# Performance work log

Measured on AMD Instinct MI355X. Metric: run time of the kernel, lower is better.

Reference implementation:

```python
import jax, jax.numpy as jnp
import numpy as np

ENCODED_DIM = 64
NUM_ENCODED = 512
BETA = 0.25


def setup_inputs() -> dict:
    key = jax.random.key(0)
    k1, k2 = jax.random.split(key)
    inputs = jax.random.normal(k1, (32, 64, 64, ENCODED_DIM), dtype=jnp.float32)
    # tf.random_uniform_initializer default: U[-0.05, 0.05]
    codebook = jax.random.uniform(k2, (ENCODED_DIM, NUM_ENCODED), dtype=jnp.float32,
                                  minval=-0.05, maxval=0.05)
    return {"inputs": inputs, "codebook": codebook}


def reference(inputs, codebook):
    original_shape = inputs.shape
    flat = inputs.reshape(-1, ENCODED_DIM)  # [N, D]
    # Squared Euclidean distances to each codebook column: [N, K]
    norms = (jnp.sum(flat ** 2, axis=1, keepdims=True)
             + jnp.sum(codebook ** 2, axis=0)
             - 2.0 * flat @ codebook)
    idx = jnp.argmin(norms, axis=1)  # [N]
    # one_hot @ codebook.T is exactly a row-gather of codebook.T
    quantized = jnp.take(codebook.T, idx, axis=0).reshape(original_shape)
    quantized_loss = jnp.mean((quantized - jax.lax.stop_gradient(inputs)) ** 2)
    commitment_loss = jnp.mean((jax.lax.stop_gradient(quantized) - inputs) ** 2)
    loss = BETA * commitment_loss + quantized_loss
    out = inputs + jax.lax.stop_gradient(quantized - inputs)
    return out, loss
```

## Files before the change

### kernel.cpp

```cpp
#include <hip/hip_runtime.h>
#include <math.h>

#define D 64
#define K 512
#define ROWS 131072
#define NELEM (ROWS * D)
#define TGAP 64.0f
#define FLAGBIT (1 << 30)

typedef _Float16 half8 __attribute__((ext_vector_type(8)));
typedef float floatx4 __attribute__((ext_vector_type(4)));


__global__ __launch_bounds__(512) void vq_setup(const float* __restrict__ cb,
                                                _Float16* __restrict__ gH,
                                                _Float16* __restrict__ gL,
                                                float* __restrict__ Bn) {
    int idx = blockIdx.x * 512 + threadIdx.x;
    int k = idx >> 9, n = idx & 511;
    float c = cb[idx];
    float t = c * 4096.0f;
    _Float16 ch = (_Float16)t;
    float r = t - (float)ch;
    _Float16 cl = (_Float16)(r * 4096.0f);
    int off = (((n >> 4) * 2 + (k >> 5)) * 64 + ((k >> 3) & 3) * 16 + (n & 15)) * 8 + (k & 7);
    gH[off] = ch;
    gL[off] = cl;
    if (blockIdx.x == 0) {
#pragma clang fp contract(off)
        int j = threadIdx.x;
        float b = 0.f;
        for (int kk = 0; kk < D; ++kk) { float cc = cb[kk * K + j]; b = b + cc * cc; }
        Bn[j] = b * 0x1p20f;
    }
}

__global__ __launch_bounds__(256, 2) void vq_main(const float* __restrict__ x,
                                                  const float* __restrict__ cb,
                                                  const _Float16* __restrict__ gH,
                                                  const _Float16* __restrict__ gL,
                                                  const float* __restrict__ Bn,
                                                  float* __restrict__ out,
                                                  double* __restrict__ loss_acc,
                                                  unsigned int* __restrict__ bitmap) {
    __shared__ float ldsB[K];
    __shared__ int rowinfo[4][64];
    __shared__ unsigned int flagbits[8];
    __shared__ float wavesum[4];

    const int tid = threadIdx.x;
    const int lane = tid & 63;
    const int w = tid >> 6;
    const int quad = lane >> 4;
    const int nn = lane & 15;

    ldsB[tid] = Bn[tid];
    ldsB[tid + 256] = Bn[tid + 256];
    if (tid < 8) flagbits[tid] = 0;

    const int rowBase = blockIdx.x * 256 + w * 64;

    half8 xh[4][2], xl[4][2];
    #pragma unroll
    for (int tt = 0; tt < 4; ++tt) {
        #pragma unroll
        for (int s = 0; s < 2; ++s) {
            const float* xp = x + (size_t)(rowBase + tt * 16 + nn) * D + s * 32 + quad * 8;
            float4 v0 = *(const float4*)xp;
            float4 v1 = *(const float4*)(xp + 4);
            float vv[8] = {v0.x, v0.y, v0.z, v0.w, v1.x, v1.y, v1.z, v1.w};
            #pragma unroll
            for (int j = 0; j < 8; ++j) {
                float t = vv[j] * 256.0f;
                _Float16 h = (_Float16)t;
                float r = t - (float)h;
                xh[tt][s][j] = h;
                xl[tt][s][j] = (_Float16)(r * 4096.0f);
            }
        }
    }
    __syncthreads();

    float m1[4][4], m2[4][4];
    int   i1[4][4];
    #pragma unroll
    for (int tt = 0; tt < 4; ++tt)
        #pragma unroll
        for (int r = 0; r < 4; ++r) { m1[tt][r] = INFINITY; m2[tt][r] = INFINITY; i1[tt][r] = 0; }

    const half8* bHp = (const half8*)gH;
    const half8* bLp = (const half8*)gL;

    #pragma unroll 2
    for (int t = 0; t < 32; ++t) {
        half8 bh0 = bHp[(t * 2 + 0) * 64 + lane];
        half8 bl0 = bLp[(t * 2 + 0) * 64 + lane];
        half8 bh1 = bHp[(t * 2 + 1) * 64 + lane];
        half8 bl1 = bLp[(t * 2 + 1) * 64 + lane];
        int col = t * 16 + nn;
        float Bj = ldsB[col];
        #pragma unroll
        for (int tt = 0; tt < 4; ++tt) {
            floatx4 a1 = {0.f, 0.f, 0.f, 0.f};
            floatx4 a2 = {0.f, 0.f, 0.f, 0.f};
            a2 = __builtin_amdgcn_mfma_f32_16x16x32_f16(xl[tt][0], bh0, a2, 0, 0, 0);
            a2 = __builtin_amdgcn_mfma_f32_16x16x32_f16(xh[tt][0], bl0, a2, 0, 0, 0);
            a1 = __builtin_amdgcn_mfma_f32_16x16x32_f16(xh[tt][0], bh0, a1, 0, 0, 0);
            a2 = __builtin_amdgcn_mfma_f32_16x16x32_f16(xl[tt][1], bh1, a2, 0, 0, 0);
            a2 = __builtin_amdgcn_mfma_f32_16x16x32_f16(xh[tt][1], bl1, a2, 0, 0, 0);
            a1 = __builtin_amdgcn_mfma_f32_16x16x32_f16(xh[tt][1], bh1, a1, 0, 0, 0);
            #pragma unroll
            for (int r = 0; r < 4; ++r) {
                float macc = fmaf(0x1p-12f, a2[r], a1[r]);
                float g = fmaf(-2.0f, macc, Bj);
                float old1 = m1[tt][r];
                bool c1 = g < old1;
                m2[tt][r] = fminf(fmaxf(g, old1), m2[tt][r]);
                m1[tt][r] = c1 ? g : old1;
                i1[tt][r] = c1 ? col : i1[tt][r];
            }
        }
    }

    #pragma unroll
    for (int dlt = 1; dlt < 16; dlt <<= 1) {
        #pragma unroll
        for (int tt = 0; tt < 4; ++tt)
            #pragma unroll
            for (int r = 0; r < 4; ++r) {
                float om1 = __shfl_xor(m1[tt][r], dlt);
                int   oi1 = __shfl_xor(i1[tt][r], dlt);
                float om2 = __shfl_xor(m2[tt][r], dlt);
                bool ofirst = (om1 < m1[tt][r]) || (om1 == m1[tt][r] && oi1 < i1[tt][r]);
                float l1   = ofirst ? m1[tt][r] : om1;
                float cand = ofirst ? om2 : m2[tt][r];
                m1[tt][r] = ofirst ? om1 : m1[tt][r];
                i1[tt][r] = ofirst ? oi1 : i1[tt][r];
                m2[tt][r] = fminf(cand, l1);
            }
    }

    if (nn == 0) {
        #pragma unroll
        for (int tt = 0; tt < 4; ++tt)
            #pragma unroll
            for (int r = 0; r < 4; ++r) {
                int rl = tt * 16 + quad * 4 + r;
                bool flg = (m2[tt][r] - m1[tt][r]) < TGAP;
                rowinfo[w][rl] = i1[tt][r] | (flg ? FLAGBIT : 0);
                if (flg) atomicOr(&flagbits[(w * 64 + rl) >> 5], 1u << ((w * 64 + rl) & 31));
            }
    }
    __syncthreads();
    if (tid < 8) bitmap[blockIdx.x * 8 + tid] = flagbits[tid];

    float lsum = 0.f;
    #pragma unroll
    for (int tt = 0; tt < 4; ++tt) {
        #pragma unroll
        for (int p = 0; p < 4; ++p) {
            int rl = tt * 16 + p * 4 + quad;
            int info = rowinfo[w][rl];
            if (!(info & FLAGBIT)) {
                int j = info & 511;
                int kb = nn * 4;
                float q0 = cb[(kb + 0) * K + j];
                float q1 = cb[(kb + 1) * K + j];
                float q2 = cb[(kb + 2) * K + j];
                float q3 = cb[(kb + 3) * K + j];
                size_t row = (size_t)rowBase + rl;
                float4 xv = *(const float4*)(x + row * D + kb);
                float e0 = q0 - xv.x, e1 = q1 - xv.y, e2 = q2 - xv.z, e3 = q3 - xv.w;
                lsum += e0 * e0 + e1 * e1 + e2 * e2 + e3 * e3;
                *(float4*)(out + row * D + kb) = make_float4(q0, q1, q2, q3);
            }
        }
    }
    #pragma unroll
    for (int off = 32; off > 0; off >>= 1) lsum += __shfl_down(lsum, off);
    if (lane == 0) wavesum[w] = lsum;
    __syncthreads();
    if (tid == 0) {
        double tot = (double)wavesum[0] + (double)wavesum[1]
                   + (double)wavesum[2] + (double)wavesum[3];
        atomicAdd(loss_acc, tot);
    }
}

__global__ __launch_bounds__(256) void vq_rescan(const float* __restrict__ x,
                                                 const float* __restrict__ cb,
                                                 float* __restrict__ out,
                                                 double* __restrict__ loss_acc,
                                                 const unsigned int* __restrict__ bitmap) {
#pragma clang fp contract(off)
    const int lane = threadIdx.x & 63;
    const int gwave = blockIdx.x * 4 + (threadIdx.x >> 6);

    unsigned int w0 = bitmap[gwave * 2 + 0];
    unsigned int w1 = bitmap[gwave * 2 + 1];
    unsigned long long mask = ((unsigned long long)w1 << 32) | w0;
    float wloss = 0.f;
    if (mask) {
        float bn[8];
        #pragma unroll
        for (int m = 0; m < 8; ++m) bn[m] = 0.f;
        for (int k = 0; k < D; ++k) {
            const float* crow = cb + k * K + lane;
            #pragma unroll
            for (int m = 0; m < 8; ++m) {
                float c = crow[m * 64];
                bn[m] = bn[m] + c * c;
            }
        }
        while (mask) {
            int b = __builtin_ctzll(mask);
            mask &= mask - 1;
            int row = gwave * 64 + b;
            const float* xr = x + (size_t)row * D;
            float A0;
            {
                float rr[8];
                #pragma unroll
                for (int l = 0; l < 8; ++l) rr[l] = xr[l] * xr[l];
                #pragma unroll
                for (int m = 1; m < 8; ++m)
                    #pragma unroll
                    for (int l = 0; l < 8; ++l) {
                        float q = xr[8 * m + l] * xr[8 * m + l];
                        rr[l] = rr[l] + q;
                    }
                A0 = ((rr[0] + rr[1]) + (rr[2] + rr[3])) + ((rr[4] + rr[5]) + (rr[6] + rr[7]));
            }
            float a[8];
            #pragma unroll
            for (int m = 0; m < 8; ++m) a[m] = 0.f;
            for (int k = 0; k < D; ++k) {
                float xk = xr[k];
                const float* crow = cb + k * K + lane;
                #pragma unroll
                for (int m = 0; m < 8; ++m)
                    a[m] = fmaf(xk, crow[m * 64], a[m]);
            }
            float db = INFINITY; int jb = 0x7fffffff;
            #pragma unroll
            for (int m = 0; m < 8; ++m) {
                float s = A0 + bn[m];
                float t2 = 2.0f * a[m];
                float d = s - t2;
                int j = lane + (m << 6);
                if (d < db) { db = d; jb = j; }
            }
            for (int s = 1; s < 64; s <<= 1) {
                float od = __shfl_xor(db, s);
                int oj = __shfl_xor(jb, s);
                if ((od < db) || (od == db && oj < jb)) { db = od; jb = oj; }
            }
            float q = cb[lane * K + jb];
            out[(size_t)row * D + lane] = q;
            float e = q - xr[lane];
            wloss += e * e;
        }
    }
    #pragma unroll
    for (int off = 32; off > 0; off >>= 1) wloss += __shfl_down(wloss, off);
    if (lane == 0 && wloss != 0.f) atomicAdd(loss_acc, (double)wloss);
}

__global__ void vq_finalize(const double* __restrict__ acc, float* __restrict__ out) {
    out[NELEM] = (float)(acc[0] * (1.25 / (double)NELEM));
}

extern "C" void kernel_launch(void* const* d_in, const int* in_sizes, int n_in,
                              void* d_out, int out_size, void* d_ws, size_t ws_size,
                              hipStream_t stream) {
    const float* x  = (const float*)d_in[0];
    const float* cb = (const float*)d_in[1];
    float* out = (float*)d_out;
    double* loss_acc = (double*)d_ws;
    float* Bn        = (float*)((char*)d_ws + 4096);
    _Float16* gH     = (_Float16*)((char*)d_ws + 8192);
    _Float16* gL     = (_Float16*)((char*)d_ws + 73728);
    unsigned int* bm = (unsigned int*)((char*)d_ws + 139264);

    hipMemsetAsync(d_ws, 0, 16, stream);
    vq_setup<<<64, 512, 0, stream>>>(cb, gH, gL, Bn);
    vq_main<<<ROWS / 256, 256, 0, stream>>>(x, cb, gH, gL, Bn, out, loss_acc, bm);
    vq_rescan<<<512, 256, 0, stream>>>(x, cb, out, loss_acc, bm);
    vq_finalize<<<1, 1, 0, stream>>>(loss_acc, out);
}
```

Baseline: 176.7 us.

## Fuse rescan and finalize into main VQ kernel with packed-index max argmin

Removes the separate rescan and finalize kernels and the memset. Each block now re-checks its own ambiguous rows in-block, and the last block to finish, tracked by an atomic counter, writes the loss. The argmin becomes a max over negated distances, with the bias preloaded into the MFMA accumulator and the column index packed into the low mantissa bits, which drops the separate index and compare registers. Blocks shrink to 128 rows with higher occupancy (launch bounds 4). In exchange, the rescan work is serialized on wave 0 of each block, and the packed index loses 9 mantissa bits of distance precision, which the widened gap threshold has to cover.

```diff
diff --git a/kernel.cpp b/kernel.cpp
--- a/kernel.cpp
+++ b/kernel.cpp
@@ -5,7 +5,8 @@
 #define K 512
 #define ROWS 131072
 #define NELEM (ROWS * D)
-#define TGAP 64.0f
+#define NBLOCKS 1024
+#define TGAP_ACC 640.0f
 #define FLAGBIT (1 << 30)
 
 typedef _Float16 half8 __attribute__((ext_vector_type(8)));
@@ -15,14 +16,16 @@
 __global__ __launch_bounds__(512) void vq_setup(const float* __restrict__ cb,
                                                 _Float16* __restrict__ gH,
                                                 _Float16* __restrict__ gL,
-                                                float* __restrict__ Bn) {
+                                                float* __restrict__ Bneg,
+                                                double* __restrict__ loss,
+                                                int* __restrict__ done) {
     int idx = blockIdx.x * 512 + threadIdx.x;
     int k = idx >> 9, n = idx & 511;
     float c = cb[idx];
     float t = c * 4096.0f;
     _Float16 ch = (_Float16)t;
     float r = t - (float)ch;
-    _Float16 cl = (_Float16)(r * 4096.0f);
+    _Float16 cl = (_Float16)r;
     int off = (((n >> 4) * 2 + (k >> 5)) * 64 + ((k >> 3) & 3) * 16 + (n & 15)) * 8 + (k & 7);
     gH[off] = ch;
     gL[off] = cl;
@@ -31,21 +34,72 @@
         int j = threadIdx.x;
         float b = 0.f;
         for (int kk = 0; kk < D; ++kk) { float cc = cb[kk * K + j]; b = b + cc * cc; }
-        Bn[j] = b * 0x1p20f;
-    }
-}
-
-__global__ __launch_bounds__(256, 2) void vq_main(const float* __restrict__ x,
+        Bneg[j] = b * -0x1p19f;
+        if (j == 0) { *loss = 0.0; *done = 0; }
+    }
+}
+
+__device__ __noinline__ void exact_row(int row, const float* __restrict__ x,
+                                       const float* __restrict__ cb,
+                                       const float* bn, int lane,
+                                       float* __restrict__ out, float& lsum) {
+#pragma clang fp contract(off)
+    const float* xr = x + (size_t)row * D;
+    float A0;
+    {
+        float rr[8];
+        #pragma unroll
+        for (int l = 0; l < 8; ++l) rr[l] = xr[l] * xr[l];
+        #pragma unroll
+        for (int m = 1; m < 8; ++m)
+            #pragma unroll
+            for (int l = 0; l < 8; ++l) {
+                float q = xr[8 * m + l] * xr[8 * m + l];
+                rr[l] = rr[l] + q;
+            }
+        A0 = ((rr[0] + rr[1]) + (rr[2] + rr[3])) + ((rr[4] + rr[5]) + (rr[6] + rr[7]));
+    }
+    float a[8];
+    #pragma unroll
+    for (int m = 0; m < 8; ++m) a[m] = 0.f;
+    for (int k = 0; k < D; ++k) {
+        float xk = xr[k];
+        const float* crow = cb + k * K + lane;
+        #pragma unroll
+        for (int m = 0; m < 8; ++m)
+            a[m] = fmaf(xk, crow[m * 64], a[m]);
+    }
+    float db = INFINITY; int jb = 0x7fffffff;
+    #pragma unroll
+    for (int m = 0; m < 8; ++m) {
+        float s = A0 + bn[m];
+        float t2 = 2.0f * a[m];
+        float d = s - t2;
+        int j = lane + (m << 6);
+        if (d < db) { db = d; jb = j; }
+    }
+    for (int s = 1; s < 64; s <<= 1) {
+        float od = __shfl_xor(db, s);
+        int oj = __shfl_xor(jb, s);
+        if ((od < db) || (od == db && oj < jb)) { db = od; jb = oj; }
+    }
+    float q = cb[lane * K + jb];
+    out[(size_t)row * D + lane] = q;
+    float e = q - xr[lane];
+    lsum += e * e;
+}
+
+__global__ __launch_bounds__(256, 4) void vq_main(const float* __restrict__ x,
                                                   const float* __restrict__ cb,
                                                   const _Float16* __restrict__ gH,
                                                   const _Float16* __restrict__ gL,
-                                                  const float* __restrict__ Bn,
+                                                  const float* __restrict__ BnegG,
                                                   float* __restrict__ out,
                                                   double* __restrict__ loss_acc,
-                                                  unsigned int* __restrict__ bitmap) {
+                                                  int* __restrict__ done) {
     __shared__ float ldsB[K];
-    __shared__ int rowinfo[4][64];
-    __shared__ unsigned int flagbits[8];
+    __shared__ int rowinfo[4][32];
+    __shared__ unsigned int flagbits[4];
     __shared__ float wavesum[4];
 
     const int tid = threadIdx.x;
@@ -54,15 +108,15 @@
     const int quad = lane >> 4;
     const int nn = lane & 15;
 
-    ldsB[tid] = Bn[tid];
-    ldsB[tid + 256] = Bn[tid + 256];
-    if (tid < 8) flagbits[tid] = 0;
-
-    const int rowBase = blockIdx.x * 256 + w * 64;
-
-    half8 xh[4][2], xl[4][2];
-    #pragma unroll
-    for (int tt = 0; tt < 4; ++tt) {
+    ldsB[tid] = BnegG[tid];
+    ldsB[tid + 256] = BnegG[tid + 256];
+    if (tid < 4) flagbits[tid] = 0;
+
+    const int rowBase = blockIdx.x * 128 + w * 32;
+
+    half8 xh[2][2], xl[2][2];
+    #pragma unroll
+    for (int tt = 0; tt < 2; ++tt) {
         #pragma unroll
         for (int s = 0; s < 2; ++s) {
             const float* xp = x + (size_t)(rowBase + tt * 16 + nn) * D + s * 32 + quad * 8;
@@ -75,18 +129,17 @@
                 _Float16 h = (_Float16)t;
                 float r = t - (float)h;
                 xh[tt][s][j] = h;
-                xl[tt][s][j] = (_Float16)(r * 4096.0f);
+                xl[tt][s][j] = (_Float16)r;
             }
         }
     }
     __syncthreads();
 
-    float m1[4][4], m2[4][4];
-    int   i1[4][4];
-    #pragma unroll
-    for (int tt = 0; tt < 4; ++tt)
-        #pragma unroll
-        for (int r = 0; r < 4; ++r) { m1[tt][r] = INFINITY; m2[tt][r] = INFINITY; i1[tt][r] = 0; }
+    float M1[2][4], M2[2][4];
+    #pragma unroll
+    for (int tt = 0; tt < 2; ++tt)
+        #pragma unroll
+        for (int r = 0; r < 4; ++r) { M1[tt][r] = -INFINITY; M2[tt][r] = -INFINITY; }
 
     const half8* bHp = (const half8*)gH;
     const half8* bLp = (const half8*)gL;
@@ -97,27 +150,23 @@
         half8 bl0 = bLp[(t * 2 + 0) * 64 + lane];
         half8 bh1 = bHp[(t * 2 + 1) * 64 + lane];
         half8 bl1 = bLp[(t * 2 + 1) * 64 + lane];
-        int col = t * 16 + nn;
-        float Bj = ldsB[col];
-        #pragma unroll
-        for (int tt = 0; tt < 4; ++tt) {
-            floatx4 a1 = {0.f, 0.f, 0.f, 0.f};
-            floatx4 a2 = {0.f, 0.f, 0.f, 0.f};
-            a2 = __builtin_amdgcn_mfma_f32_16x16x32_f16(xl[tt][0], bh0, a2, 0, 0, 0);
-            a2 = __builtin_amdgcn_mfma_f32_16x16x32_f16(xh[tt][0], bl0, a2, 0, 0, 0);
-            a1 = __builtin_amdgcn_mfma_f32_16x16x32_f16(xh[tt][0], bh0, a1, 0, 0, 0);
-            a2 = __builtin_amdgcn_mfma_f32_16x16x32_f16(xl[tt][1], bh1, a2, 0, 0, 0);
-            a2 = __builtin_amdgcn_mfma_f32_16x16x32_f16(xh[tt][1], bl1, a2, 0, 0, 0);
-            a1 = __builtin_amdgcn_mfma_f32_16x16x32_f16(xh[tt][1], bh1, a1, 0, 0, 0);
+        float bneg = ldsB[t * 16 + nn];
+        unsigned int colbits = (unsigned)(t * 16 + nn);
+        #pragma unroll
+        for (int tt = 0; tt < 2; ++tt) {
+            floatx4 acc = {bneg, bneg, bneg, bneg};
+            acc = __builtin_amdgcn_mfma_f32_16x16x32_f16(xh[tt][0], bh0, acc, 0, 0, 0);
+            acc = __builtin_amdgcn_mfma_f32_16x16x32_f16(xl[tt][0], bh0, acc, 0, 0, 0);
+            acc = __builtin_amdgcn_mfma_f32_16x16x32_f16(xh[tt][0], bl0, acc, 0, 0, 0);
+            acc = __builtin_amdgcn_mfma_f32_16x16x32_f16(xh[tt][1], bh1, acc, 0, 0, 0);
+            acc = __builtin_amdgcn_mfma_f32_16x16x32_f16(xl[tt][1], bh1, acc, 0, 0, 0);
+            acc = __builtin_amdgcn_mfma_f32_16x16x32_f16(xh[tt][1], bl1, acc, 0, 0, 0);
             #pragma unroll
             for (int r = 0; r < 4; ++r) {
-                float macc = fmaf(0x1p-12f, a2[r], a1[r]);
-                float g = fmaf(-2.0f, macc, Bj);
-                float old1 = m1[tt][r];
-                bool c1 = g < old1;
-                m2[tt][r] = fminf(fmaxf(g, old1), m2[tt][r]);
-                m1[tt][r] = c1 ? g : old1;
-                i1[tt][r] = c1 ? col : i1[tt][r];
+                float gq = __uint_as_float((__float_as_uint(acc[r]) & ~511u) | colbits);
+                float lo = fminf(M1[tt][r], gq);
+                M2[tt][r] = fmaxf(M2[tt][r], lo);
+                M1[tt][r] = fmaxf(M1[tt][r], gq);
             }
         }
     }
@@ -125,38 +174,34 @@
     #pragma unroll
     for (int dlt = 1; dlt < 16; dlt <<= 1) {
         #pragma unroll
-        for (int tt = 0; tt < 4; ++tt)
+        for (int tt = 0; tt < 2; ++tt)
             #pragma unroll
             for (int r = 0; r < 4; ++r) {
-                float om1 = __shfl_xor(m1[tt][r], dlt);
-                int   oi1 = __shfl_xor(i1[tt][r], dlt);
-                float om2 = __shfl_xor(m2[tt][r], dlt);
-                bool ofirst = (om1 < m1[tt][r]) || (om1 == m1[tt][r] && oi1 < i1[tt][r]);
-                float l1   = ofirst ? m1[tt][r] : om1;
-                float cand = ofirst ? om2 : m2[tt][r];
-                m1[tt][r] = ofirst ? om1 : m1[tt][r];
-                i1[tt][r] = ofirst ? oi1 : i1[tt][r];
-                m2[tt][r] = fminf(cand, l1);
+                float o1 = __shfl_xor(M1[tt][r], dlt);
+                float o2 = __shfl_xor(M2[tt][r], dlt);
+                float lo = fminf(M1[tt][r], o1);
+                M1[tt][r] = fmaxf(M1[tt][r], o1);
+                M2[tt][r] = fmaxf(fmaxf(M2[tt][r], o2), lo);
             }
     }
 
     if (nn == 0) {
         #pragma unroll
-        for (int tt = 0; tt < 4; ++tt)
+        for (int tt = 0; tt < 2; ++tt)
             #pragma unroll
             for (int r = 0; r < 4; ++r) {
                 int rl = tt * 16 + quad * 4 + r;
-                bool flg = (m2[tt][r] - m1[tt][r]) < TGAP;
-                rowinfo[w][rl] = i1[tt][r] | (flg ? FLAGBIT : 0);
-                if (flg) atomicOr(&flagbits[(w * 64 + rl) >> 5], 1u << ((w * 64 + rl) & 31));
+                int col = (int)(__float_as_uint(M1[tt][r]) & 511u);
+                bool flg = (M1[tt][r] - M2[tt][r]) < TGAP_ACC;
+                rowinfo[w][rl] = col | (flg ? FLAGBIT : 0);
+                if (flg) atomicOr(&flagbits[w], 1u << rl);
             }
     }
     __syncthreads();
-    if (tid < 8) bitmap[blockIdx.x * 8 + tid] = flagbits[tid];
 
     float lsum = 0.f;
     #pragma unroll
-    for (int tt = 0; tt < 4; ++tt) {
+    for (int tt = 0; tt < 2; ++tt) {
         #pragma unroll
         for (int p = 0; p < 4; ++p) {
             int rl = tt * 16 + p * 4 + quad;
@@ -168,7 +213,7 @@
                 float q1 = cb[(kb + 1) * K + j];
                 float q2 = cb[(kb + 2) * K + j];
                 float q3 = cb[(kb + 3) * K + j];
-                size_t row = (size_t)rowBase + rl;
+                size_t row = (size_t)blockIdx.x * 128 + w * 32 + rl;
                 float4 xv = *(const float4*)(x + row * D + kb);
                 float e0 = q0 - xv.x, e1 = q1 - xv.y, e2 = q2 - xv.z, e3 = q3 - xv.w;
                 lsum += e0 * e0 + e1 * e1 + e2 * e2 + e3 * e3;
@@ -176,6 +221,36 @@
             }
         }
     }
+
+    if (w == 0) {
+        unsigned int any = flagbits[0] | flagbits[1] | flagbits[2] | flagbits[3];
+        if (any) {
+            float bn[8];
+            {
+#pragma clang fp contract(off)
+                #pragma unroll
+                for (int m = 0; m < 8; ++m) bn[m] = 0.f;
+                for (int k = 0; k < D; ++k) {
+                    const float* crow = cb + k * K + lane;
+                    #pragma unroll
+                    for (int m = 0; m < 8; ++m) {
+                        float c = crow[m * 64];
+                        bn[m] = bn[m] + c * c;
+                    }
+                }
+            }
+            for (int wd = 0; wd < 4; ++wd) {
+                unsigned int mask = flagbits[wd];
+                while (mask) {
+                    int b = __builtin_ctz(mask);
+                    mask &= mask - 1;
+                    int row = blockIdx.x * 128 + wd * 32 + b;
+                    exact_row(row, x, cb, bn, lane, out, lsum);
+                }
+            }
+        }
+    }
+
     #pragma unroll
     for (int off = 32; off > 0; off >>= 1) lsum += __shfl_down(lsum, off);
     if (lane == 0) wavesum[w] = lsum;
@@ -184,90 +259,13 @@
         double tot = (double)wavesum[0] + (double)wavesum[1]
                    + (double)wavesum[2] + (double)wavesum[3];
         atomicAdd(loss_acc, tot);
-    }
-}
-
-__global__ __launch_bounds__(256) void vq_rescan(const float* __restrict__ x,
-                                                 const float* __restrict__ cb,
-                                                 float* __restrict__ out,
-                                                 double* __restrict__ loss_acc,
-                                                 const unsigned int* __restrict__ bitmap) {
-#pragma clang fp contract(off)
-    const int lane = threadIdx.x & 63;
-    const int gwave = blockIdx.x * 4 + (threadIdx.x >> 6);
-
-    unsigned int w0 = bitmap[gwave * 2 + 0];
-    unsigned int w1 = bitmap[gwave * 2 + 1];
-    unsigned long long mask = ((unsigned long long)w1 << 32) | w0;
-    float wloss = 0.f;
-    if (mask) {
-        float bn[8];
-        #pragma unroll
-        for (int m = 0; m < 8; ++m) bn[m] = 0.f;
-        for (int k = 0; k < D; ++k) {
-            const float* crow = cb + k * K + lane;
-            #pragma unroll
-            for (int m = 0; m < 8; ++m) {
-                float c = crow[m * 64];
-                bn[m] = bn[m] + c * c;
-            }
-        }
-        while (mask) {
-            int b = __builtin_ctzll(mask);
-            mask &= mask - 1;
-            int row = gwave * 64 + b;
-            const float* xr = x + (size_t)row * D;
-            float A0;
-            {
-                float rr[8];
-                #pragma unroll
-                for (int l = 0; l < 8; ++l) rr[l] = xr[l] * xr[l];
-                #pragma unroll
-                for (int m = 1; m < 8; ++m)
-                    #pragma unroll
-                    for (int l = 0; l < 8; ++l) {
-                        float q = xr[8 * m + l] * xr[8 * m + l];
-                        rr[l] = rr[l] + q;
-                    }
-                A0 = ((rr[0] + rr[1]) + (rr[2] + rr[3])) + ((rr[4] + rr[5]) + (rr[6] + rr[7]));
-            }
-            float a[8];
-            #pragma unroll
-            for (int m = 0; m < 8; ++m) a[m] = 0.f;
-            for (int k = 0; k < D; ++k) {
-                float xk = xr[k];
-                const float* crow = cb + k * K + lane;
-                #pragma unroll
-                for (int m = 0; m < 8; ++m)
-                    a[m] = fmaf(xk, crow[m * 64], a[m]);
-            }
-            float db = INFINITY; int jb = 0x7fffffff;
-            #pragma unroll
-            for (int m = 0; m < 8; ++m) {
-                float s = A0 + bn[m];
-                float t2 = 2.0f * a[m];
-                float d = s - t2;
-                int j = lane + (m << 6);
-                if (d < db) { db = d; jb = j; }
-            }
-            for (int s = 1; s < 64; s <<= 1) {
-                float od = __shfl_xor(db, s);
-                int oj = __shfl_xor(jb, s);
-                if ((od < db) || (od == db && oj < jb)) { db = od; jb = oj; }
-            }
-            float q = cb[lane * K + jb];
-            out[(size_t)row * D + lane] = q;
-            float e = q - xr[lane];
-            wloss += e * e;
-        }
-    }
-    #pragma unroll
-    for (int off = 32; off > 0; off >>= 1) wloss += __shfl_down(wloss, off);
-    if (lane == 0 && wloss != 0.f) atomicAdd(loss_acc, (double)wloss);
-}
-
-__global__ void vq_finalize(const double* __restrict__ acc, float* __restrict__ out) {
-    out[NELEM] = (float)(acc[0] * (1.25 / (double)NELEM));
+        __threadfence();
+        int old = atomicAdd(done, 1);
+        if (old == NBLOCKS - 1) {
+            double total = atomicAdd(loss_acc, 0.0);
+            out[NELEM] = (float)(total * (1.25 / (double)NELEM));
+        }
+    }
 }
 
 extern "C" void kernel_launch(void* const* d_in, const int* in_sizes, int n_in,
@@ -277,14 +275,11 @@
     const float* cb = (const float*)d_in[1];
     float* out = (float*)d_out;
     double* loss_acc = (double*)d_ws;
-    float* Bn        = (float*)((char*)d_ws + 4096);
+    int* done        = (int*)((char*)d_ws + 8);
+    float* Bneg      = (float*)((char*)d_ws + 4096);
     _Float16* gH     = (_Float16*)((char*)d_ws + 8192);
     _Float16* gL     = (_Float16*)((char*)d_ws + 73728);
-    unsigned int* bm = (unsigned int*)((char*)d_ws + 139264);
-
-    hipMemsetAsync(d_ws, 0, 16, stream);
-    vq_setup<<<64, 512, 0, stream>>>(cb, gH, gL, Bn);
-    vq_main<<<ROWS / 256, 256, 0, stream>>>(x, cb, gH, gL, Bn, out, loss_acc, bm);
-    vq_rescan<<<512, 256, 0, stream>>>(x, cb, out, loss_acc, bm);
-    vq_finalize<<<1, 1, 0, stream>>>(loss_acc, out);
-}
+
+    vq_setup<<<64, 512, 0, stream>>>(cb, gH, gL, Bneg, loss_acc, done);
+    vq_main<<<NBLOCKS, 256, 0, stream>>>(x, cb, gH, gL, Bneg, out, loss_acc, done);
+}
```

Result: slower. 276.3 us (+56.4%).
